# Performance work log

Hardware: AMD Instinct MI355X
Metric: run time of the kernel (lower is better)

The kernel has to match this reference:

```python
import jax, jax.numpy as jnp
import numpy as np

DIM = 512
NUM_HEADS = 8
HEAD_DIM = DIM // NUM_HEADS
SCALE = HEAD_DIM ** -0.5


def setup_inputs() -> dict:
    key = jax.random.key(0)
    ks = jax.random.split(key, 11)
    B, T, D = 2, 4096, DIM
    s = 0.02
    return {
        "query": jax.random.normal(ks[0], (B, T, D), jnp.float32),
        "key_": jax.random.normal(ks[1], (B, T, D), jnp.float32),
        "value": jax.random.normal(ks[2], (B, T, D), jnp.float32),
        "Wq": jax.random.normal(ks[3], (D, D), jnp.float32) * s,
        "bq": jnp.zeros((D,), jnp.float32),
        "Wk": jax.random.normal(ks[4], (D, D), jnp.float32) * s,
        "bk": jnp.zeros((D,), jnp.float32),
        "Wv": jax.random.normal(ks[5], (D, D), jnp.float32) * s,
        "bv": jnp.zeros((D,), jnp.float32),
        "Wo": jax.random.normal(ks[6], (D, D), jnp.float32) * s,
        "bo": jnp.zeros((D,), jnp.float32),
    }


def reference(query, key_, value, Wq, bq, Wk, bk, Wv, bv, Wo, bo):
    B, T, D = query.shape
    H, Hd = NUM_HEADS, HEAD_DIM
    # Linear projections (torch Linear: x @ W.T + b)
    q = (query @ Wq.T + bq).reshape(B, T, H, Hd).transpose(0, 2, 1, 3)   # [B,H,T,Hd]
    k = (key_ @ Wk.T + bk).reshape(B, -1, H, Hd).transpose(0, 2, 1, 3)    # [B,H,S,Hd]
    v = (value @ Wv.T + bv).reshape(B, -1, H, Hd).transpose(0, 2, 1, 3)   # [B,H,S,Hd]
    # Full O(T*S) score matrix, as in the original (non-fused) module
    scores = jnp.einsum("bhtd,bhsd->bhts", q, k) * SCALE                  # [B,H,T,S]
    weights = jax.nn.softmax(scores, axis=-1)
    out = jnp.einsum("bhts,bhsd->bhtd", weights, v)                       # [B,H,T,Hd]
    out = out.transpose(0, 2, 1, 3).reshape(B, T, D)
    return out @ Wo.T + bo
```

## Files before the change

### kernel.cpp

```cpp
#include <hip/hip_runtime.h>
#include <cstdint>
#include <cstddef>

typedef __attribute__((ext_vector_type(8)))  __bf16 bf16x8;
typedef __attribute__((ext_vector_type(4)))  float  f32x4;
typedef __attribute__((ext_vector_type(16))) float  f32x16;
typedef __attribute__((ext_vector_type(8)))  unsigned short us8;

#define MFMA(a, b, c)   __builtin_amdgcn_mfma_f32_16x16x32_bf16((a), (b), (c), 0, 0, 0)
#define MFMA32(a, b, c) __builtin_amdgcn_mfma_f32_32x32x16_bf16((a), (b), (c), 0, 0, 0)

#define QSCALE 0.18033688011112042f

__device__ __forceinline__ unsigned short f2bf(float f) {
  unsigned u = __float_as_uint(f);
  u += 0x7fffu + ((u >> 16) & 1u);
  return (unsigned short)(u >> 16);
}

__device__ __forceinline__ float bf2f(unsigned short s) {
  unsigned u = ((unsigned)s) << 16;
  return __uint_as_float(u);
}

__device__ __forceinline__ unsigned pk2bf(float lo, float hi) {
  unsigned a = __float_as_uint(lo) + 0x8000u;
  unsigned b = __float_as_uint(hi) + 0x8000u;
  return __builtin_amdgcn_perm(b, a, 0x07060302u);
}

__device__ __forceinline__ void pl32swap(unsigned& a, unsigned& b) {
  asm("v_permlane32_swap_b32 %0, %1" : "+v"(a), "+v"(b));
}

__device__ __forceinline__ void gload16(const void* g, void* l) {
  __builtin_amdgcn_global_load_lds(
      (__attribute__((address_space(1))) unsigned int*)(uintptr_t)g,
      (__attribute__((address_space(3))) unsigned int*)l,
      16, 0, 0);
}

__device__ __forceinline__ float tree16(const float* p) {
  float a = (p[0] + p[1]) + (p[2] + p[3]);
  float b = (p[4] + p[5]) + (p[6] + p[7]);
  float c = (p[8] + p[9]) + (p[10] + p[11]);
  float d = (p[12] + p[13]) + (p[14] + p[15]);
  return (a + b) + (c + d);
}

struct CastArgs {
  const float*    src[7];
  unsigned short* dst[7];
  int             n4[7];
};
__global__ __launch_bounds__(256) void cast_kernel(CastArgs a) {
  int z = blockIdx.y;
  const float* __restrict__ in = a.src[z];
  unsigned short* __restrict__ out = a.dst[z];
  int i = blockIdx.x * 256 + threadIdx.x;
  if (i < a.n4[z]) {
    float4 f = ((const float4*)in)[i];
    ushort4 r;
    r.x = f2bf(f.x); r.y = f2bf(f.y); r.z = f2bf(f.z); r.w = f2bf(f.w);
    ((ushort4*)out)[i] = r;
  }
}

struct ProjArgs {
  const unsigned short* X[3];
  const unsigned short* W[3];
  const float*          bias[3];
  unsigned short*       out[3];
};

__global__ __launch_bounds__(256) void proj_qkv_kernel(ProjArgs args) {
  __shared__ alignas(16) unsigned short smem[16384];

  const int z = blockIdx.z;
  const unsigned short* __restrict__ X   = args.X[z];
  const unsigned short* __restrict__ W   = args.W[z];
  const float* __restrict__ bias         = args.bias[z];
  unsigned short* __restrict__ out       = args.out[z];
  const float scl = (z == 0) ? QSCALE : 1.0f;

  const int t = threadIdx.x;
  const int w = t >> 6, lane = t & 63;
  const int quad = lane >> 4, l15 = lane & 15;
  const int wr = w >> 1, wc = w & 1;
  const int m0 = blockIdx.x * 128, n0 = blockIdx.y * 128;

  const int srow = t >> 2;
  const int scol = (((t & 3) ^ (srow & 3)) << 3);

  f32x4 acc[4][4] = {};

  {
    unsigned short* sA = smem;
    unsigned short* sB = smem + 4096;
    gload16(X + (size_t)(m0 + srow) * 512 + scol,      &sA[w * 512]);
    gload16(X + (size_t)(m0 + srow + 64) * 512 + scol, &sA[2048 + w * 512]);
    gload16(W + (size_t)(n0 + srow) * 512 + scol,      &sB[w * 512]);
    gload16(W + (size_t)(n0 + srow + 64) * 512 + scol, &sB[2048 + w * 512]);
  }

  for (int k0 = 0; k0 < 512; k0 += 32) {
    const int buf = (k0 >> 5) & 1;
    unsigned short* sA = smem + buf * 8192;
    unsigned short* sB = sA + 4096;
    if (k0 < 480) {
      unsigned short* nA = smem + (buf ^ 1) * 8192;
      unsigned short* nB = nA + 4096;
      const int kn = k0 + 32;
      gload16(X + (size_t)(m0 + srow) * 512 + kn + scol,      &nA[w * 512]);
      gload16(X + (size_t)(m0 + srow + 64) * 512 + kn + scol, &nA[2048 + w * 512]);
      gload16(W + (size_t)(n0 + srow) * 512 + kn + scol,      &nB[w * 512]);
      gload16(W + (size_t)(n0 + srow + 64) * 512 + kn + scol, &nB[2048 + w * 512]);
      asm volatile("s_waitcnt vmcnt(4)" ::: "memory");
    } else {
      asm volatile("s_waitcnt vmcnt(0)" ::: "memory");
    }
    __builtin_amdgcn_s_barrier();
    asm volatile("" ::: "memory");

    bf16x8 af[4], bfr[4];
#pragma unroll
    for (int mt = 0; mt < 4; ++mt) {
      int ra = wr * 64 + mt * 16 + l15;
      af[mt] = *(const bf16x8*)&sA[ra * 32 + ((quad ^ (ra & 3)) << 3)];
    }
#pragma unroll
    for (int nt = 0; nt < 4; ++nt) {
      int rb = wc * 64 + nt * 16 + l15;
      bfr[nt] = *(const bf16x8*)&sB[rb * 32 + ((quad ^ (rb & 3)) << 3)];
    }
#pragma unroll
    for (int mt = 0; mt < 4; ++mt)
#pragma unroll
      for (int nt = 0; nt < 4; ++nt)
        acc[mt][nt] = MFMA(af[mt], bfr[nt], acc[mt][nt]);

    asm volatile("" ::: "memory");
    __builtin_amdgcn_s_barrier();
  }

  if (z != 2) {
#pragma unroll
    for (int nt = 0; nt < 4; ++nt) {
      int n = n0 + wc * 64 + nt * 16 + l15;
      float bv = bias[n];
      int h = n >> 6, hd = n & 63;
#pragma unroll
      for (int mt = 0; mt < 4; ++mt) {
#pragma unroll
        for (int r = 0; r < 4; ++r) {
          int m = m0 + wr * 64 + mt * 16 + quad * 4 + r;
          int b = m >> 12, tt = m & 4095;
          out[(((size_t)(b * 8 + h)) * 4096 + tt) * 64 + hd] =
              f2bf((acc[mt][nt][r] + bv) * scl);
        }
      }
    }
  } else {
    const int b   = m0 >> 12;
    const int tt0 = m0 & 4095;
#pragma unroll
    for (int h2 = 0; h2 < 2; ++h2) {
      __syncthreads();
      if (wc == h2) {
#pragma unroll
        for (int nt = 0; nt < 4; ++nt) {
          int nl = nt * 16 + l15;
          float bv = bias[n0 + h2 * 64 + nl];
#pragma unroll
          for (int mt = 0; mt < 4; ++mt)
#pragma unroll
            for (int r = 0; r < 4; ++r) {
              int ml = wr * 64 + mt * 16 + quad * 4 + r;
              smem[nl * 136 + ml] = f2bf((acc[mt][nt][r] + bv) * scl);
            }
        }
      }
      __syncthreads();
      const int row = t >> 2;
      const int c4  = (t & 3) * 8;
      const int n   = n0 + h2 * 64 + row;
      unsigned short* dst = out + ((size_t)(b * 512 + n)) * 4096 + tt0;
#pragma unroll
      for (int k = 0; k < 4; ++k)
        *(us8*)(dst + c4 + k * 32) = *(const us8*)&smem[row * 136 + c4 + k * 32];
    }
  }
}

__global__ __launch_bounds__(256) void proj_out_kernel(
    const unsigned short* __restrict__ X, const unsigned short* __restrict__ W,
    const float* __restrict__ bias, float* __restrict__ out) {
  __shared__ alignas(16) unsigned short smem[16384];

  const int t = threadIdx.x;
  const int w = t >> 6, lane = t & 63;
  const int quad = lane >> 4, l15 = lane & 15;
  const int wr = w >> 1, wc = w & 1;
  const int m0 = blockIdx.x * 128, n0 = blockIdx.y * 128;
  const int srow = t >> 2;
  const int scol = (((t & 3) ^ (srow & 3)) << 3);

  f32x4 acc[4][4] = {};

  {
    unsigned short* sA = smem;
    unsigned short* sB = smem + 4096;
    gload16(X + (size_t)(m0 + srow) * 512 + scol,      &sA[w * 512]);
    gload16(X + (size_t)(m0 + srow + 64) * 512 + scol, &sA[2048 + w * 512]);
    gload16(W + (size_t)(n0 + srow) * 512 + scol,      &sB[w * 512]);
    gload16(W + (size_t)(n0 + srow + 64) * 512 + scol, &sB[2048 + w * 512]);
  }

  for (int k0 = 0; k0 < 512; k0 += 32) {
    const int buf = (k0 >> 5) & 1;
    unsigned short* sA = smem + buf * 8192;
    unsigned short* sB = sA + 4096;
    if (k0 < 480) {
      unsigned short* nA = smem + (buf ^ 1) * 8192;
      unsigned short* nB = nA + 4096;
      const int kn = k0 + 32;
      gload16(X + (size_t)(m0 + srow) * 512 + kn + scol,      &nA[w * 512]);
      gload16(X + (size_t)(m0 + srow + 64) * 512 + kn + scol, &nA[2048 + w * 512]);
      gload16(W + (size_t)(n0 + srow) * 512 + kn + scol,      &nB[w * 512]);
      gload16(W + (size_t)(n0 + srow + 64) * 512 + kn + scol, &nB[2048 + w * 512]);
      asm volatile("s_waitcnt vmcnt(4)" ::: "memory");
    } else {
      asm volatile("s_waitcnt vmcnt(0)" ::: "memory");
    }
    __builtin_amdgcn_s_barrier();
    asm volatile("" ::: "memory");

    bf16x8 af[4], bfr[4];
#pragma unroll
    for (int mt = 0; mt < 4; ++mt) {
      int ra = wr * 64 + mt * 16 + l15;
      af[mt] = *(const bf16x8*)&sA[ra * 32 + ((quad ^ (ra & 3)) << 3)];
    }
#pragma unroll
    for (int nt = 0; nt < 4; ++nt) {
      int rb = wc * 64 + nt * 16 + l15;
      bfr[nt] = *(const bf16x8*)&sB[rb * 32 + ((quad ^ (rb & 3)) << 3)];
    }
#pragma unroll
    for (int mt = 0; mt < 4; ++mt)
#pragma unroll
      for (int nt = 0; nt < 4; ++nt)
        acc[mt][nt] = MFMA(af[mt], bfr[nt], acc[mt][nt]);

    asm volatile("" ::: "memory");
    __builtin_amdgcn_s_barrier();
  }

#pragma unroll
  for (int nt = 0; nt < 4; ++nt) {
    int n = n0 + wc * 64 + nt * 16 + l15;
    float bv = bias[n];
#pragma unroll
    for (int mt = 0; mt < 4; ++mt) {
#pragma unroll
      for (int r = 0; r < 4; ++r) {
        int m = m0 + wr * 64 + mt * 16 + quad * 4 + r;
        out[(size_t)m * 512 + n] = acc[mt][nt][r] + bv;
      }
    }
  }
}

__global__ __launch_bounds__(128, 2) void attn_kernel(
    const unsigned short* __restrict__ Q, const unsigned short* __restrict__ K,
    const unsigned short* __restrict__ VT,
    unsigned short* __restrict__ pO0, unsigned short* __restrict__ pO1,
    float* __restrict__ pL) {
  __shared__ alignas(16) unsigned short kt[2][4096];
  __shared__ alignas(16) unsigned short vt[2][4096];

  const int t = threadIdx.x;
  const int w = t >> 6;
  const int lane = t & 63;
  const int l31 = lane & 31, h = lane >> 5;

  const int wg  = blockIdx.x + gridDim.x * blockIdx.y;
  const int swz = (wg & 7) * 128 + (wg >> 3);
  const int qt  = swz & 31;
  const int bh2 = swz >> 5;
  const int bh  = bh2 & 15, half = bh2 >> 4;

  const unsigned short* __restrict__ Qp  = Q  + (size_t)bh * 4096 * 64;
  const unsigned short* __restrict__ Kp  = K  + (size_t)bh * 4096 * 64;
  const unsigned short* __restrict__ VTp = VT + (size_t)bh * 64 * 4096;

  const int q0w = qt * 128 + w * 64;
  const int sbase = half * 2048;

  const int lr   = lane >> 3;
  const int gcol = (((lane & 7) ^ lr) << 3);

#define STAGE(bbuf, s0)                                                        \
  {                                                                            \
    _Pragma("unroll")                                                          \
    for (int i = 0; i < 4; ++i)                                                \
      gload16(Kp + (size_t)((s0) + w * 32 + i * 8 + lr) * 64 + gcol,           \
              &kt[bbuf][(w * 32 + i * 8) * 64]);                               \
    _Pragma("unroll")                                                          \
    for (int i = 0; i < 4; ++i)                                                \
      gload16(VTp + (size_t)(w * 32 + i * 8 + lr) * 4096 + (s0) + gcol,        \
              &vt[bbuf][(w * 32 + i * 8) * 64]);                               \
  }

  STAGE(0, sbase);

  bf16x8 aqA[4], aqB[4];
#pragma unroll
  for (int kd = 0; kd < 4; ++kd) {
    aqA[kd] = *(const bf16x8*)(Qp + (size_t)(q0w + l31) * 64 + kd * 16 + h * 8);
    aqB[kd] = *(const bf16x8*)(Qp + (size_t)(q0w + 32 + l31) * 64 + kd * 16 + h * 8);
  }

  f32x16 o0a = {}, o1a = {}, o0b = {}, o1b = {};
  float lia = 0.f, lib = 0.f;

  const int swzk = l31 & 7;

  for (int j = 0; j < 32; ++j) {
    const int cb = j & 1, nb = cb ^ 1;
    if (j < 31) {
      STAGE(nb, sbase + (j + 1) * 64);
      asm volatile("s_waitcnt vmcnt(8)" ::: "memory");
    } else {
      asm volatile("s_waitcnt vmcnt(0)" ::: "memory");
    }
    __builtin_amdgcn_s_barrier();
    asm volatile("" ::: "memory");

    const unsigned short* ktb = kt[cb];
    const unsigned short* vtb = vt[cb];

#pragma unroll
    for (int st = 0; st < 2; ++st) {
      bf16x8 kf[4];
#pragma unroll
      for (int kd = 0; kd < 4; ++kd)
        kf[kd] = *(const bf16x8*)&ktb[(st * 32 + l31) * 64 +
                                      (((2 * kd + h) ^ swzk) << 3)];
      f32x16 sa = {}, sb = {};
#pragma unroll
      for (int kd = 0; kd < 4; ++kd) {
        sa = MFMA32(kf[kd], aqA[kd], sa);
        sb = MFMA32(kf[kd], aqB[kd], sb);
      }

      float pA[16], pB[16];
#pragma unroll
      for (int r = 0; r < 16; ++r) {
        pA[r] = __builtin_amdgcn_exp2f(sa[r]);
        pB[r] = __builtin_amdgcn_exp2f(sb[r]);
      }
      lia += tree16(pA);
      lib += tree16(pB);

      unsigned XgA[4], YgA[4], XgB[4], YgB[4];
#pragma unroll
      for (int g = 0; g < 4; ++g) {
        XgA[g] = pk2bf(pA[4 * g + 0], pA[4 * g + 1]);
        YgA[g] = pk2bf(pA[4 * g + 2], pA[4 * g + 3]);
        XgB[g] = pk2bf(pB[4 * g + 0], pB[4 * g + 1]);
        YgB[g] = pk2bf(pB[4 * g + 2], pB[4 * g + 3]);
      }

#pragma unroll
      for (int ks = 0; ks < 2; ++ks) {
        const int c = st * 4 + 2 * ks + h;
        bf16x8 v0 = *(const bf16x8*)&vtb[l31 * 64 + ((c ^ swzk) << 3)];
        bf16x8 v1 = *(const bf16x8*)&vtb[(l31 + 32) * 64 + ((c ^ swzk) << 3)];

        unsigned a0 = XgA[2 * ks], a2 = XgA[2 * ks + 1];
        unsigned a1 = YgA[2 * ks], a3 = YgA[2 * ks + 1];
        pl32swap(a0, a2);
        pl32swap(a1, a3);
        union { unsigned u[4]; bf16x8 v; } paA;
        paA.u[0] = a0; paA.u[1] = a1; paA.u[2] = a2; paA.u[3] = a3;
        o0a = MFMA32(paA.v, v0, o0a);
        o1a = MFMA32(paA.v, v1, o1a);

        unsigned b0 = XgB[2 * ks], b2 = XgB[2 * ks + 1];
        unsigned b1 = YgB[2 * ks], b3 = YgB[2 * ks + 1];
        pl32swap(b0, b2);
        pl32swap(b1, b3);
        union { unsigned u[4]; bf16x8 v; } paB;
        paB.u[0] = b0; paB.u[1] = b1; paB.u[2] = b2; paB.u[3] = b3;
        o0b = MFMA32(paB.v, v0, o0b);
        o1b = MFMA32(paB.v, v1, o1b);
      }
    }

    asm volatile("" ::: "memory");
    __builtin_amdgcn_s_barrier();
  }
#undef STAGE

  lia += __shfl_xor(lia, 32, 64);
  lib += __shfl_xor(lib, 32, 64);
  float* __restrict__ PLh = pL + half * 65536 + bh * 4096;
  if (h == 0) {
    PLh[q0w + l31]      = lia;
    PLh[q0w + 32 + l31] = lib;
  }

  unsigned short* __restrict__ PO = half ? pO1 : pO0;
  const int bq = bh >> 3, hh = bh & 7;
#pragma unroll
  for (int r = 0; r < 16; ++r) {
    const int qloc = (r & 3) + 8 * (r >> 2) + 4 * h;
    const size_t baseA = ((size_t)bq * 4096 + q0w + qloc) * 512 + hh * 64;
    PO[baseA + l31]      = f2bf(o0a[r]);
    PO[baseA + 32 + l31] = f2bf(o1a[r]);
    const size_t baseB = ((size_t)bq * 4096 + q0w + 32 + qloc) * 512 + hh * 64;
    PO[baseB + l31]      = f2bf(o0b[r]);
    PO[baseB + 32 + l31] = f2bf(o1b[r]);
  }
}

__global__ __launch_bounds__(256) void combine_kernel(
    const unsigned short* __restrict__ p0, const unsigned short* __restrict__ p1,
    const float* __restrict__ pL, unsigned short* __restrict__ ao) {
  const int i = blockIdx.x * 256 + threadIdx.x;
  const int idx8 = i * 8;
  const int col = idx8 & 511;
  const int t   = (idx8 >> 9) & 4095;
  const int bq  = idx8 >> 21;
  const int bh  = bq * 8 + (col >> 6);
  const float inv = 1.0f / (pL[bh * 4096 + t] + pL[65536 + bh * 4096 + t]);
  us8 a = *(const us8*)&p0[idx8];
  us8 b = *(const us8*)&p1[idx8];
  us8 o;
#pragma unroll
  for (int k = 0; k < 8; ++k)
    o[k] = f2bf((bf2f(a[k]) + bf2f(b[k])) * inv);
  *(us8*)&ao[idx8] = o;
}

extern "C" void kernel_launch(void* const* d_in, const int* in_sizes, int n_in,
                              void* d_out, int out_size, void* d_ws, size_t ws_size,
                              hipStream_t stream) {
  (void)in_sizes; (void)n_in; (void)out_size; (void)ws_size;
  const float* query = (const float*)d_in[0];
  const float* key_  = (const float*)d_in[1];
  const float* value = (const float*)d_in[2];
  const float* Wq = (const float*)d_in[3];
  const float* bq = (const float*)d_in[4];
  const float* Wk = (const float*)d_in[5];
  const float* bk = (const float*)d_in[6];
  const float* Wv = (const float*)d_in[7];
  const float* bv = (const float*)d_in[8];
  const float* Wo = (const float*)d_in[9];
  const float* bo = (const float*)d_in[10];
  float* out = (float*)d_out;

  char* ws = (char*)d_ws;
  const size_t MB = 1024 * 1024;
  unsigned short* Xq  = (unsigned short*)(ws + 0 * MB);
  unsigned short* Xk  = (unsigned short*)(ws + 8 * MB);
  unsigned short* Xv  = (unsigned short*)(ws + 16 * MB);
  unsigned short* Wqb = (unsigned short*)(ws + 24 * MB);
  unsigned short* Wkb = (unsigned short*)(ws + 24 * MB + 512 * 1024);
  unsigned short* Wvb = (unsigned short*)(ws + 25 * MB);
  unsigned short* qb  = (unsigned short*)(ws + 26 * MB);
  unsigned short* kb  = (unsigned short*)(ws + 34 * MB);
  unsigned short* vtb = (unsigned short*)(ws + 42 * MB);
  unsigned short* Wob = (unsigned short*)(ws + 58 * MB);
  unsigned short* pO0 = (unsigned short*)(ws + 0 * MB);
  unsigned short* pO1 = (unsigned short*)(ws + 9 * MB);
  float*          pL  = (float*)(ws + 18 * MB);
  unsigned short* ao  = (unsigned short*)(ws + 42 * MB);

  CastArgs ca;
  ca.src[0] = query; ca.src[1] = key_; ca.src[2] = value;
  ca.src[3] = Wq;    ca.src[4] = Wk;   ca.src[5] = Wv;  ca.src[6] = Wo;
  ca.dst[0] = Xq;    ca.dst[1] = Xk;   ca.dst[2] = Xv;
  ca.dst[3] = Wqb;   ca.dst[4] = Wkb;  ca.dst[5] = Wvb; ca.dst[6] = Wob;
  ca.n4[0] = ca.n4[1] = ca.n4[2] = 1048576;
  ca.n4[3] = ca.n4[4] = ca.n4[5] = ca.n4[6] = 65536;
  cast_kernel<<<dim3(4096, 7), 256, 0, stream>>>(ca);

  ProjArgs pa;
  pa.X[0] = Xq;  pa.X[1] = Xk;  pa.X[2] = Xv;
  pa.W[0] = Wqb; pa.W[1] = Wkb; pa.W[2] = Wvb;
  pa.bias[0] = bq; pa.bias[1] = bk; pa.bias[2] = bv;
  pa.out[0] = qb; pa.out[1] = kb; pa.out[2] = vtb;
  proj_qkv_kernel<<<dim3(64, 4, 3), 256, 0, stream>>>(pa);

  attn_kernel<<<dim3(32, 32), 128, 0, stream>>>(qb, kb, vtb, pO0, pO1, pL);

  combine_kernel<<<dim3(2048), 256, 0, stream>>>(pO0, pO1, pL, ao);

  proj_out_kernel<<<dim3(64, 4), 256, 0, stream>>>(ao, Wob, bo, out);
}
```

Measured before the change: 236.1 us.

## Fuse split-KV combine into output projection and use hardware bf16 pack

```diff
diff --git a/kernel.cpp b/kernel.cpp
--- a/kernel.cpp
+++ b/kernel.cpp
@@ -23,10 +23,10 @@
   return __uint_as_float(u);
 }
 
-__device__ __forceinline__ unsigned pk2bf(float lo, float hi) {
-  unsigned a = __float_as_uint(lo) + 0x8000u;
-  unsigned b = __float_as_uint(hi) + 0x8000u;
-  return __builtin_amdgcn_perm(b, a, 0x07060302u);
+__device__ __forceinline__ unsigned cvtpk(float lo, float hi) {
+  unsigned r;
+  asm("v_cvt_pk_bf16_f32 %0, %1, %2" : "=v"(r) : "v"(lo), "v"(hi));
+  return r;
 }
 
 __device__ __forceinline__ void pl32swap(unsigned& a, unsigned& b) {
@@ -193,78 +193,106 @@
 }
 
 __global__ __launch_bounds__(256) void proj_out_kernel(
-    const unsigned short* __restrict__ X, const unsigned short* __restrict__ W,
+    const unsigned short* __restrict__ P0, const unsigned short* __restrict__ P1,
+    const float* __restrict__ pL, const unsigned short* __restrict__ W,
     const float* __restrict__ bias, float* __restrict__ out) {
-  __shared__ alignas(16) unsigned short smem[16384];
+  __shared__ alignas(16) unsigned short sA[2][2048];
+  __shared__ alignas(16) unsigned short sB[2][4096];
+  __shared__ float invL[512];
 
   const int t = threadIdx.x;
   const int w = t >> 6, lane = t & 63;
   const int quad = lane >> 4, l15 = lane & 15;
-  const int wr = w >> 1, wc = w & 1;
-  const int m0 = blockIdx.x * 128, n0 = blockIdx.y * 128;
+  const int m0 = blockIdx.x * 64, n0 = blockIdx.y * 128;
+  const int b  = m0 >> 12, tt0 = m0 & 4095;
+
+  {
+    const int hh = t >> 5;
+    const int r2 = (t & 31) * 2;
+#pragma unroll
+    for (int i = 0; i < 2; ++i) {
+      const int row = r2 + i;
+      const size_t ix = (size_t)(b * 8 + hh) * 4096 + tt0 + row;
+      invL[hh * 64 + row] = 1.0f / (pL[ix] + pL[65536 + ix]);
+    }
+  }
+
+  const int arow = t >> 2, ac = t & 3;
   const int srow = t >> 2;
   const int scol = (((t & 3) ^ (srow & 3)) << 3);
 
-  f32x4 acc[4][4] = {};
+  __syncthreads();
 
   {
-    unsigned short* sA = smem;
-    unsigned short* sB = smem + 4096;
-    gload16(X + (size_t)(m0 + srow) * 512 + scol,      &sA[w * 512]);
-    gload16(X + (size_t)(m0 + srow + 64) * 512 + scol, &sA[2048 + w * 512]);
-    gload16(W + (size_t)(n0 + srow) * 512 + scol,      &sB[w * 512]);
-    gload16(W + (size_t)(n0 + srow + 64) * 512 + scol, &sB[2048 + w * 512]);
-  }
+    us8 a0 = *(const us8*)&P0[(size_t)(m0 + arow) * 512 + ac * 8];
+    us8 a1 = *(const us8*)&P1[(size_t)(m0 + arow) * 512 + ac * 8];
+    const float inv = invL[arow];
+    unsigned o[4];
+#pragma unroll
+    for (int i = 0; i < 4; ++i)
+      o[i] = cvtpk((bf2f(a0[2 * i]) + bf2f(a1[2 * i])) * inv,
+                   (bf2f(a0[2 * i + 1]) + bf2f(a1[2 * i + 1])) * inv);
+    *(us8*)&sA[0][arow * 32 + ((ac ^ (arow & 3)) << 3)] = *(us8*)o;
+    gload16(W + (size_t)(n0 + srow) * 512 + scol,      &sB[0][w * 512]);
+    gload16(W + (size_t)(n0 + srow + 64) * 512 + scol, &sB[0][2048 + w * 512]);
+  }
+  __syncthreads();
+
+  f32x4 acc[4][2] = {};
 
   for (int k0 = 0; k0 < 512; k0 += 32) {
     const int buf = (k0 >> 5) & 1;
-    unsigned short* sA = smem + buf * 8192;
-    unsigned short* sB = sA + 4096;
+
+    us8 a0n = {}, a1n = {};
+    float invn = 0.f;
     if (k0 < 480) {
-      unsigned short* nA = smem + (buf ^ 1) * 8192;
-      unsigned short* nB = nA + 4096;
       const int kn = k0 + 32;
-      gload16(X + (size_t)(m0 + srow) * 512 + kn + scol,      &nA[w * 512]);
-      gload16(X + (size_t)(m0 + srow + 64) * 512 + kn + scol, &nA[2048 + w * 512]);
-      gload16(W + (size_t)(n0 + srow) * 512 + kn + scol,      &nB[w * 512]);
-      gload16(W + (size_t)(n0 + srow + 64) * 512 + kn + scol, &nB[2048 + w * 512]);
-      asm volatile("s_waitcnt vmcnt(4)" ::: "memory");
-    } else {
-      asm volatile("s_waitcnt vmcnt(0)" ::: "memory");
-    }
+      a0n = *(const us8*)&P0[(size_t)(m0 + arow) * 512 + kn + ac * 8];
+      a1n = *(const us8*)&P1[(size_t)(m0 + arow) * 512 + kn + ac * 8];
+      invn = invL[(kn >> 6) * 64 + arow];
+      gload16(W + (size_t)(n0 + srow) * 512 + kn + scol,      &sB[buf ^ 1][w * 512]);
+      gload16(W + (size_t)(n0 + srow + 64) * 512 + kn + scol, &sB[buf ^ 1][2048 + w * 512]);
+    }
+
+    bf16x8 af[4], bfr[2];
+#pragma unroll
+    for (int mt = 0; mt < 4; ++mt) {
+      int ra = mt * 16 + l15;
+      af[mt] = *(const bf16x8*)&sA[buf][ra * 32 + ((quad ^ (ra & 3)) << 3)];
+    }
+#pragma unroll
+    for (int nt = 0; nt < 2; ++nt) {
+      int rb = w * 32 + nt * 16 + l15;
+      bfr[nt] = *(const bf16x8*)&sB[buf][rb * 32 + ((quad ^ (rb & 3)) << 3)];
+    }
+#pragma unroll
+    for (int mt = 0; mt < 4; ++mt)
+#pragma unroll
+      for (int nt = 0; nt < 2; ++nt)
+        acc[mt][nt] = MFMA(af[mt], bfr[nt], acc[mt][nt]);
+
+    if (k0 < 480) {
+      unsigned o[4];
+#pragma unroll
+      for (int i = 0; i < 4; ++i)
+        o[i] = cvtpk((bf2f(a0n[2 * i]) + bf2f(a1n[2 * i])) * invn,
+                     (bf2f(a0n[2 * i + 1]) + bf2f(a1n[2 * i + 1])) * invn);
+      *(us8*)&sA[buf ^ 1][arow * 32 + ((ac ^ (arow & 3)) << 3)] = *(us8*)o;
+    }
+
+    asm volatile("s_waitcnt vmcnt(0) lgkmcnt(0)" ::: "memory");
     __builtin_amdgcn_s_barrier();
-    asm volatile("" ::: "memory");
-
-    bf16x8 af[4], bfr[4];
+  }
+
+#pragma unroll
+  for (int nt = 0; nt < 2; ++nt) {
+    int n = n0 + w * 32 + nt * 16 + l15;
+    float bv = bias[n];
 #pragma unroll
     for (int mt = 0; mt < 4; ++mt) {
-      int ra = wr * 64 + mt * 16 + l15;
-      af[mt] = *(const bf16x8*)&sA[ra * 32 + ((quad ^ (ra & 3)) << 3)];
-    }
-#pragma unroll
-    for (int nt = 0; nt < 4; ++nt) {
-      int rb = wc * 64 + nt * 16 + l15;
-      bfr[nt] = *(const bf16x8*)&sB[rb * 32 + ((quad ^ (rb & 3)) << 3)];
-    }
-#pragma unroll
-    for (int mt = 0; mt < 4; ++mt)
-#pragma unroll
-      for (int nt = 0; nt < 4; ++nt)
-        acc[mt][nt] = MFMA(af[mt], bfr[nt], acc[mt][nt]);
-
-    asm volatile("" ::: "memory");
-    __builtin_amdgcn_s_barrier();
-  }
-
-#pragma unroll
-  for (int nt = 0; nt < 4; ++nt) {
-    int n = n0 + wc * 64 + nt * 16 + l15;
-    float bv = bias[n];
-#pragma unroll
-    for (int mt = 0; mt < 4; ++mt) {
 #pragma unroll
       for (int r = 0; r < 4; ++r) {
-        int m = m0 + wr * 64 + mt * 16 + quad * 4 + r;
+        int m = m0 + mt * 16 + quad * 4 + r;
         out[(size_t)m * 512 + n] = acc[mt][nt][r] + bv;
       }
     }
@@ -366,10 +394,10 @@
       unsigned XgA[4], YgA[4], XgB[4], YgB[4];
 #pragma unroll
       for (int g = 0; g < 4; ++g) {
-        XgA[g] = pk2bf(pA[4 * g + 0], pA[4 * g + 1]);
-        YgA[g] = pk2bf(pA[4 * g + 2], pA[4 * g + 3]);
-        XgB[g] = pk2bf(pB[4 * g + 0], pB[4 * g + 1]);
-        YgB[g] = pk2bf(pB[4 * g + 2], pB[4 * g + 3]);
+        XgA[g] = cvtpk(pA[4 * g + 0], pA[4 * g + 1]);
+        YgA[g] = cvtpk(pA[4 * g + 2], pA[4 * g + 3]);
+        XgB[g] = cvtpk(pB[4 * g + 0], pB[4 * g + 1]);
+        YgB[g] = cvtpk(pB[4 * g + 2], pB[4 * g + 3]);
       }
 
 #pragma unroll
@@ -423,25 +451,6 @@
     PO[baseB + l31]      = f2bf(o0b[r]);
     PO[baseB + 32 + l31] = f2bf(o1b[r]);
   }
-}
-
-__global__ __launch_bounds__(256) void combine_kernel(
-    const unsigned short* __restrict__ p0, const unsigned short* __restrict__ p1,
-    const float* __restrict__ pL, unsigned short* __restrict__ ao) {
-  const int i = blockIdx.x * 256 + threadIdx.x;
-  const int idx8 = i * 8;
-  const int col = idx8 & 511;
-  const int t   = (idx8 >> 9) & 4095;
-  const int bq  = idx8 >> 21;
-  const int bh  = bq * 8 + (col >> 6);
-  const float inv = 1.0f / (pL[bh * 4096 + t] + pL[65536 + bh * 4096 + t]);
-  us8 a = *(const us8*)&p0[idx8];
-  us8 b = *(const us8*)&p1[idx8];
-  us8 o;
-#pragma unroll
-  for (int k = 0; k < 8; ++k)
-    o[k] = f2bf((bf2f(a[k]) + bf2f(b[k])) * inv);
-  *(us8*)&ao[idx8] = o;
 }
 
 extern "C" void kernel_launch(void* const* d_in, const int* in_sizes, int n_in,
@@ -476,7 +485,6 @@
   unsigned short* pO0 = (unsigned short*)(ws + 0 * MB);
   unsigned short* pO1 = (unsigned short*)(ws + 9 * MB);
   float*          pL  = (float*)(ws + 18 * MB);
-  unsigned short* ao  = (unsigned short*)(ws + 42 * MB);
 
   CastArgs ca;
   ca.src[0] = query; ca.src[1] = key_; ca.src[2] = value;
@@ -496,7 +504,5 @@
 
   attn_kernel<<<dim3(32, 32), 128, 0, stream>>>(qb, kb, vtb, pO0, pO1, pL);
 
-  combine_kernel<<<dim3(2048), 256, 0, stream>>>(pO0, pO1, pL, ao);
-
-  proj_out_kernel<<<dim3(64, 4), 256, 0, stream>>>(ao, Wob, bo, out);
-}
+  proj_out_kernel<<<dim3(128, 4), 256, 0, stream>>>(pO0, pO1, pL, Wob, bo, out);
+}
```

New measurement: 220.0 us. 1.07x faster.
